# Performance work log

Hardware: AMD Instinct MI355X
Metric: run time of the kernel (lower is better)

## Reference

```python
import jax, jax.numpy as jnp
import numpy as np

E, H, NGRAM, TM, B, NB = 1024, 16, 2, 512, 4, 32


def setup_inputs() -> dict:
    key = jax.random.key(0)
    ks = jax.random.split(key, 12)
    T3 = (NGRAM + 1) * TM
    s = 0.02
    d = {}
    d["hidden_states"] = jax.random.normal(ks[0], (T3, B, E), jnp.float32)
    d["self_attn_mask"] = jax.random.normal(ks[1], (TM, TM), jnp.float32)
    d["ngram_mask_matrix"] = jax.random.normal(ks[2], (NGRAM, 1, TM, 2 * TM), jnp.float32)
    d["i_buckets_main_stream"] = jax.random.randint(ks[3], (B, TM, TM), 0, NB, jnp.int32)
    d["i_bucket_relative_stream"] = jax.random.randint(ks[4], (B, TM, 2 * TM), 0, NB, jnp.int32)
    d["Wq"] = jax.random.normal(ks[5], (E, E), jnp.float32) * s
    d["bq"] = jnp.zeros((E,), jnp.float32)
    d["Wk"] = jax.random.normal(ks[6], (E, E), jnp.float32) * s
    d["bk"] = jnp.zeros((E,), jnp.float32)
    d["Wv"] = jax.random.normal(ks[7], (E, E), jnp.float32) * s
    d["bv"] = jnp.zeros((E,), jnp.float32)
    d["Wo"] = jax.random.normal(ks[8], (E, E), jnp.float32) * s
    d["bo"] = jnp.zeros((E,), jnp.float32)
    d["Wr"] = jax.random.normal(ks[9], (NB * H, E), jnp.float32) * s
    d["br"] = jnp.zeros((NB * H,), jnp.float32)
    return d


def _lin(x, W, b):
    return x @ W.T + b


def reference(hidden_states, self_attn_mask, ngram_mask_matrix,
              i_buckets_main_stream, i_bucket_relative_stream,
              Wq, bq, Wk, bk, Wv, bv, Wo, bo, Wr, br):
    T3, Bb, Ee = hidden_states.shape
    hd = Ee // H
    Tm = T3 // (NGRAM + 1)
    BH = Bb * H

    # projections; q is pre-scaled as in the torch module
    q = _lin(hidden_states, Wq, bq) * (hd ** -0.5)
    k = _lin(hidden_states, Wk, bk)
    v = _lin(hidden_states, Wv, bv)
    # (T3, B, E) -> (BH, T3, hd)
    q = q.reshape(T3, BH, hd).transpose(1, 0, 2)
    k = k.reshape(T3, BH, hd).transpose(1, 0, 2)
    v = v.reshape(T3, BH, hd).transpose(1, 0, 2)

    q_parts = jnp.split(q, NGRAM + 1, axis=1)
    k_parts = jnp.split(k, NGRAM + 1, axis=1)
    v_parts = jnp.split(v, NGRAM + 1, axis=1)
    h_parts = jnp.split(hidden_states, NGRAM + 1, axis=0)
    q_main, k_main, v_main, h_main = q_parts[0], k_parts[0], v_parts[0], h_parts[0]

    # ---------- main stream ----------
    aw_main = jnp.einsum('btd,bsd->bts', q_main, k_main)  # (BH, Tm, Tm)

    # relative-position logits: per-query learned bucket logits, gathered by bucket id
    vals = _lin(h_main.transpose(1, 0, 2), Wr, br)          # (B, Tm, NB*H)
    vals = vals.reshape(Bb, Tm, NB, H).transpose(0, 3, 1, 2).reshape(BH, Tm, NB)
    idx = jnp.broadcast_to(i_buckets_main_stream[:, None], (Bb, H, Tm, Tm)).reshape(BH, Tm, Tm)
    aw_main = aw_main + jnp.take_along_axis(vals, idx, axis=2) + self_attn_mask

    probs_main = jax.nn.softmax(aw_main.astype(jnp.float32), axis=-1).astype(aw_main.dtype)
    attn_main = jnp.einsum('bts,bsd->btd', probs_main, v_main)   # (BH, Tm, hd)
    attn_main = attn_main.transpose(1, 0, 2).reshape(Tm, Bb, Ee)
    attn_main = _lin(attn_main, Wo, bo)                           # (Tm, B, E)

    # ---------- ngram streams ----------
    q_ng = jnp.stack(q_parts[1:], 0)                              # (N, BH, Tm, hd)
    k_ng = jnp.stack([jnp.concatenate([k_main, kp], axis=1) for kp in k_parts[1:]], 0)  # (N, BH, 2Tm, hd)
    v_ng = jnp.stack([jnp.concatenate([v_main, vp], axis=1) for vp in v_parts[1:]], 0)
    h_ng = jnp.stack(h_parts[1:], 0)                              # (N, Tm, B, E)

    aw_ng = jnp.einsum('nbtc,nbsc->nbts', q_ng, k_ng)             # (N, BH, Tm, 2Tm)

    vals_ng = _lin(h_ng.transpose(0, 2, 1, 3), Wr, br)            # (N, B, Tm, NB*H)
    vals_ng = vals_ng.reshape(NGRAM, Bb, Tm, NB, H).transpose(0, 1, 4, 2, 3).reshape(NGRAM, BH, Tm, NB)
    idx_ng = jnp.broadcast_to(i_bucket_relative_stream[None, :, None],
                              (NGRAM, Bb, H, Tm, 2 * Tm)).reshape(NGRAM, BH, Tm, 2 * Tm)
    aw_ng = aw_ng + jnp.take_along_axis(vals_ng, idx_ng, axis=-1) + ngram_mask_matrix

    probs_ng = jax.nn.softmax(aw_ng.astype(jnp.float32), axis=-1).astype(aw_ng.dtype)
    attn_ng = jnp.einsum('nbts,nbsc->nbtc', probs_ng, v_ng)       # (N, BH, Tm, hd)
    attn_ng = attn_ng.transpose(0, 2, 1, 3).reshape(NGRAM, Tm, Bb, Ee)
    attn_ng = _lin(attn_ng, Wo, bo)                                # (N, Tm, B, E)

    attn = jnp.concatenate([attn_main[None], attn_ng], axis=0).reshape(T3, Bb, Ee)
    return attn
```

## Files before the change

kernel.cpp:

```cpp
#include <hip/hip_runtime.h>
#include <hip/hip_fp16.h>
#include <cstdint>

#define T3   1536
#define TMQ  512
#define BB   4
#define EE   1024
#define HH   16
#define HD   64
#define NBK  32
#define BHH  64

#define LOG2E 1.44269504f
#define SM_SHIFT 4.0f

typedef _Float16 half8 __attribute__((ext_vector_type(8)));
typedef float    f32x4 __attribute__((ext_vector_type(4)));

#define SWZ(r, o) ((o) ^ (((r) & 7) << 4))

__device__ inline void gl_lds16(const void* g, void* l) {
    __builtin_amdgcn_global_load_lds(
        (const __attribute__((address_space(1))) uint32_t*)g,
        (__attribute__((address_space(3))) uint32_t*)l, 16, 0, 0);
}

#define VM_WAIT4() asm volatile("s_waitcnt vmcnt(4)" ::: "memory")
#define VM_WAIT0() asm volatile("s_waitcnt vmcnt(0)" ::: "memory")
#define BARRIER()  __builtin_amdgcn_s_barrier()

__global__ __launch_bounds__(256) void cvt_all(
    const float* __restrict__ hs, const float* __restrict__ Wq,
    const float* __restrict__ Wk, const float* __restrict__ Wv,
    const float* __restrict__ Wo, const float* __restrict__ Wr,
    __half* __restrict__ dst)
{
    const long i = (long)blockIdx.x * 256 + threadIdx.x;
    const float* src; long off;
    if (i < 1572864L) { src = hs; off = i; }
    else {
        const long j = i - 1572864L;
        const int  w = (int)(j >> 18);
        const long r = j & 262143L;
        src = (w == 0) ? Wq : (w == 1) ? Wk : (w == 2) ? Wv : (w == 3) ? Wo : Wr;
        off = r;
    }
    const float4 v = ((const float4*)src)[off];
    const __half2 h0 = __floats2half2_rn(v.x, v.y);
    const __half2 h1 = __floats2half2_rn(v.z, v.w);
    uint2 u;
    u.x = *(const unsigned int*)&h0;
    u.y = *(const unsigned int*)&h1;
    ((uint2*)dst)[i] = u;
}

template<int MODE>
__global__ __launch_bounds__(256) void gemm16(
    const __half* __restrict__ A,
    const __half* __restrict__ Wa, const __half* __restrict__ Wb,
    const __half* __restrict__ Wc, const __half* __restrict__ Wd,
    const float* __restrict__ ba, const float* __restrict__ bb,
    const float* __restrict__ bc, const float* __restrict__ bd,
    void* __restrict__ oa, void* __restrict__ ob,
    void* __restrict__ oc, void* __restrict__ od)
{
    __shared__ __half As0[128 * 32], Bs0[128 * 32];
    __shared__ __half As1[128 * 32], Bs1[128 * 32];

    const int tid  = threadIdx.x;
    const int w    = tid >> 6, lane = tid & 63;
    const int m0   = blockIdx.y * 128;

    const __half* Wsel; const float* bsel; void* osel;
    float scale, offs; int n0; int sel = 0;
    if (MODE == 0) {
        const int bx = blockIdx.x;
        sel  = (bx < 24) ? (bx >> 3) : 3;
        n0   = (bx < 24) ? (bx & 7) * 128 : (bx - 24) * 128;
        Wsel = sel == 0 ? Wa : (sel == 1 ? Wb : (sel == 2 ? Wc : Wd));
        bsel = sel == 0 ? ba : (sel == 1 ? bb : (sel == 2 ? bc : bd));
        osel = sel == 0 ? oa : (sel == 1 ? ob : (sel == 2 ? oc : od));
        scale = (sel == 0) ? 0.125f * LOG2E : (sel == 3 ? LOG2E : 1.0f);
        offs  = (sel == 3) ? -SM_SHIFT * LOG2E : 0.0f;
    } else {
        n0 = blockIdx.x * 128; Wsel = Wa; bsel = ba; osel = oa;
        scale = 1.0f; offs = 0.0f;
    }

    f32x4 acc[4][4];
    #pragma unroll
    for (int i = 0; i < 4; ++i)
        #pragma unroll
        for (int j = 0; j < 4; ++j) acc[i][j] = (f32x4){0.f, 0.f, 0.f, 0.f};

    const int wr = w >> 1, wc = w & 1;
    const int lrow = lane & 15, lkg = lane >> 4;
    const int aoff  = (wr * 64 + lrow) * 64;
    const int boff  = (wc * 64 + lrow) * 64;
    const int kbase = (((lkg + ((lrow & 7) >> 1)) & 3) << 4);

    const int stb0 = w * 2048, stb1 = w * 2048 + 1024;
    const int off0 = stb0 + lane * 16, off1 = stb1 + lane * 16;
    const int srow0 = off0 >> 6, srow1 = off1 >> 6;
    const int scol0 = (((((off0 >> 4) & 3) - ((srow0 & 7) >> 1)) & 3) << 4);
    const int scol1 = (((((off1 >> 4) & 3) - ((srow1 & 7) >> 1)) & 3) << 4);
    const char* Ab  = (const char*)A;
    const char* Wb8 = (const char*)Wsel;

#define STAGEK(AS, BS, K0) do {                                                   \
    gl_lds16(Ab  + (size_t)(m0 + srow0) * 2048 + (size_t)(K0) * 2 + scol0,        \
             (char*)(AS) + stb0);                                                 \
    gl_lds16(Wb8 + (size_t)(n0 + srow0) * 2048 + (size_t)(K0) * 2 + scol0,        \
             (char*)(BS) + stb0);                                                 \
    gl_lds16(Ab  + (size_t)(m0 + srow1) * 2048 + (size_t)(K0) * 2 + scol1,        \
             (char*)(AS) + stb1);                                                 \
    gl_lds16(Wb8 + (size_t)(n0 + srow1) * 2048 + (size_t)(K0) * 2 + scol1,        \
             (char*)(BS) + stb1);                                                 \
} while (0)

#define COMPUTEK(AS, BS) do {                                                     \
    half8 af[4], bf[4];                                                           \
    _Pragma("unroll")                                                             \
    for (int m = 0; m < 4; ++m)                                                   \
        af[m] = *(const half8*)((const char*)(AS) + aoff + m * 1024 + kbase);     \
    _Pragma("unroll")                                                             \
    for (int n = 0; n < 4; ++n)                                                   \
        bf[n] = *(const half8*)((const char*)(BS) + boff + n * 1024 + kbase);     \
    _Pragma("unroll")                                                             \
    for (int m = 0; m < 4; ++m)                                                   \
        _Pragma("unroll")                                                         \
        for (int n = 0; n < 4; ++n)                                               \
            acc[m][n] = __builtin_amdgcn_mfma_f32_16x16x32_f16(af[m], bf[n],      \
                                                               acc[m][n], 0, 0, 0);\
} while (0)

    STAGEK(As0, Bs0, 0);

    #pragma unroll 1
    for (int t = 0; t < 16; ++t) {
        const int k0 = t * 64;
        STAGEK(As1, Bs1, k0 + 32);
        VM_WAIT4();
        BARRIER();
        COMPUTEK(As0, Bs0);
        BARRIER();
        if (t < 15) { STAGEK(As0, Bs0, k0 + 64); VM_WAIT4(); }
        else        { VM_WAIT0(); }
        BARRIER();
        COMPUTEK(As1, Bs1);
        BARRIER();
    }

#undef STAGEK
#undef COMPUTEK

    const int col_l  = lane & 15;
    const int row_l4 = (lane >> 4) * 4;
    #pragma unroll
    for (int n = 0; n < 4; ++n) {
        const int gcol = n0 + wc * 64 + n * 16 + col_l;
        const float bias = bsel[gcol];
        #pragma unroll
        for (int m = 0; m < 4; ++m) {
            #pragma unroll
            for (int j = 0; j < 4; ++j) {
                const int grow = m0 + wr * 64 + m * 16 + row_l4 + j;
                const float cval = (acc[m][n][j] + bias) * scale + offs;
                if (MODE == 0) {
                    const int t3 = grow >> 2, bb2 = grow & 3;
                    if (sel == 3) {
                        const int st = t3 >> 9, tm = t3 & 511;
                        const int nb = gcol >> 4, hh2 = gcol & 15;
                        ((float*)osel)[(((size_t)(st * BHH + bb2 * HH + hh2)) * TMQ + tm) * NBK + nb] = cval;
                    } else {
                        const int hh2 = gcol >> 6, d = gcol & 63;
                        __half* oh = (__half*)osel;
                        const __half hv = __float2half(cval);
                        if (sel == 2)
                            oh[((size_t)((bb2 * HH + hh2) * HD + d)) * T3 + t3] = hv;
                        else
                            oh[(((size_t)(bb2 * HH + hh2)) * T3 + t3) * HD + d] = hv;
                    }
                } else {
                    ((float*)osel)[(size_t)grow * EE + gcol] = cval;
                }
            }
        }
    }
}

__global__ __launch_bounds__(256) void attn_mfma(
    const __half* __restrict__ q, const __half* __restrict__ k,
    const __half* __restrict__ vt, const float* __restrict__ vals,
    const float* __restrict__ self_mask, const float* __restrict__ ngram_mask,
    const int* __restrict__ ibm, const int* __restrict__ ibr,
    __half* __restrict__ attn_pre)
{
    __shared__ __half QP [64 * 64];
    __shared__ __half Ks [64 * 64];
    __shared__ __half Vts[64 * 64];
    __shared__ float  vals_s[64 * NBK];

    const int bid = blockIdx.x;
    const int xcd = bid & 7, rr = bid >> 3;
    int s, bh, qt;
    if (rr < 128) { const int g = xcd * 128 + rr; s = 1 + (g >> 9); bh = (g >> 3) & 63; qt = g & 7; }
    else          { const int mi = xcd * 64 + (rr - 128); s = 0; bh = mi >> 3; qt = mi & 7; }
    const int b = bh >> 4, h = bh & 15;
    const int tid = threadIdx.x;
    const int w = tid >> 6, lane = tid & 63;
    const int lc = lane & 15, lg = lane >> 4;
    const int nch = (s == 0) ? 8 : 16;

    {
        const char* qg = (const char*)(q + ((size_t)bh * T3 + s * TMQ + qt * 64) * HD);
        const char* vg = (const char*)(vals + (((size_t)s * BHH + bh) * TMQ + qt * 64) * NBK);
        #pragma unroll
        for (int p = 0; p < 2; ++p) {
            const int u = tid + p * 256;
            const int row = u >> 3, sub = (u & 7) * 16;
            *(uint4*)((char*)QP + row * 128 + SWZ(row, sub)) = *(const uint4*)(qg + (size_t)u * 16);
            *(uint4*)((char*)vals_s + (size_t)u * 16)        = *(const uint4*)(vg + (size_t)u * 16);
        }
    }

    uint4 ku0, ku1, vu0, vu1;
    int   ix[4][4];
    float mk[4][4];
    {
        const char* kg = (const char*)(k + (size_t)bh * T3 * HD);
        const char* vg = (const char*)(vt + (size_t)bh * HD * T3);
        ku0 = *(const uint4*)(kg + (size_t)tid * 16);
        ku1 = *(const uint4*)(kg + (size_t)(tid + 256) * 16);
        vu0 = *(const uint4*)(vg + (size_t)(tid >> 3) * (T3 * 2) + (tid & 7) * 16);
        vu1 = *(const uint4*)(vg + (size_t)((tid + 256) >> 3) * (T3 * 2) + (tid & 7) * 16);
        #pragma unroll
        for (int j = 0; j < 4; ++j) {
            const int t = qt * 64 + w * 16 + lg * 4 + j;
            const int* ip; const float* mp;
            if (s == 0) { ip = ibm + ((size_t)b * TMQ + t) * TMQ + lc;
                          mp = self_mask + (size_t)t * TMQ + lc; }
            else        { ip = ibr + ((size_t)b * TMQ + t) * (2 * TMQ) + lc;
                          mp = ngram_mask + ((size_t)(s - 1) * TMQ + t) * (2 * TMQ) + lc; }
            #pragma unroll
            for (int n = 0; n < 4; ++n) { ix[j][n] = ip[n * 16]; mk[j][n] = mp[n * 16]; }
        }
    }
    __syncthreads();

    half8 aq[2];
    {
        const int qr = w * 16 + lc;
        const char* qb = (const char*)QP + qr * 128;
        aq[0] = *(const half8*)(qb + SWZ(qr, lg * 16));
        aq[1] = *(const half8*)(qb + SWZ(qr, 64 + lg * 16));
    }

    f32x4 o[4];
    #pragma unroll
    for (int nd = 0; nd < 4; ++nd) o[nd] = (f32x4){0.f, 0.f, 0.f, 0.f};
    float l_p[4] = {0.f, 0.f, 0.f, 0.f};

    for (int c = 0; c < nch; ++c) {
        if (c > 0) __syncthreads();
        {
            const int u0 = tid, u1 = tid + 256;
            const int r0 = u0 >> 3, s0 = (u0 & 7) * 16;
            const int r1 = u1 >> 3, s1 = (u1 & 7) * 16;
            *(uint4*)((char*)Ks  + r0 * 128 + SWZ(r0, s0)) = ku0;
            *(uint4*)((char*)Ks  + r1 * 128 + SWZ(r1, s1)) = ku1;
            *(uint4*)((char*)Vts + r0 * 128 + SWZ(r0, s0)) = vu0;
            *(uint4*)((char*)Vts + r1 * 128 + SWZ(r1, s1)) = vu1;
        }
        __syncthreads();

        if (c + 1 < nch) {
            const int jn  = (c + 1) * 64;
            const int t3n = (jn < TMQ) ? jn : s * TMQ + (jn - TMQ);
            const char* kg = (const char*)(k + ((size_t)bh * T3 + t3n) * HD);
            const char* vg = (const char*)(vt + (size_t)bh * HD * T3 + t3n);
            ku0 = *(const uint4*)(kg + (size_t)tid * 16);
            ku1 = *(const uint4*)(kg + (size_t)(tid + 256) * 16);
            vu0 = *(const uint4*)(vg + (size_t)(tid >> 3) * (T3 * 2) + (tid & 7) * 16);
            vu1 = *(const uint4*)(vg + (size_t)((tid + 256) >> 3) * (T3 * 2) + (tid & 7) * 16);
        }

        f32x4 sc[4];
        #pragma unroll
        for (int n = 0; n < 4; ++n) sc[n] = (f32x4){0.f, 0.f, 0.f, 0.f};
        __builtin_amdgcn_s_setprio(1);
        #pragma unroll
        for (int ks = 0; ks < 2; ++ks) {
            #pragma unroll
            for (int n = 0; n < 4; ++n) {
                const int kr = n * 16 + lc;
                const half8 bk = *(const half8*)((const char*)Ks + kr * 128 + SWZ(kr, ks * 64 + lg * 16));
                sc[n] = __builtin_amdgcn_mfma_f32_16x16x32_f16(aq[ks], bk, sc[n], 0, 0, 0);
            }
        }
        __builtin_amdgcn_s_setprio(0);

        #pragma unroll
        for (int j = 0; j < 4; ++j) {
            const int ql = w * 16 + lg * 4 + j;
            const float* vr = vals_s + ql * NBK;
            float p[4];
            #pragma unroll
            for (int n = 0; n < 4; ++n) {
                const float sv = fmaf(mk[j][n], LOG2E, sc[n][j] + vr[ix[j][n]]);
                p[n] = __builtin_amdgcn_exp2f(sv);
            }
            l_p[j] += (p[0] + p[1]) + (p[2] + p[3]);
            char* pb = (char*)QP + ql * 128;
            *(__half*)(pb + SWZ(ql, (0 * 16 + lc) * 2)) = __float2half(p[0]);
            *(__half*)(pb + SWZ(ql, (1 * 16 + lc) * 2)) = __float2half(p[1]);
            *(__half*)(pb + SWZ(ql, (2 * 16 + lc) * 2)) = __float2half(p[2]);
            *(__half*)(pb + SWZ(ql, (3 * 16 + lc) * 2)) = __float2half(p[3]);
        }

        if (c + 1 < nch) {
            const int jn = (c + 1) * 64;
            #pragma unroll
            for (int j = 0; j < 4; ++j) {
                const int t = qt * 64 + w * 16 + lg * 4 + j;
                const int* ip; const float* mp;
                if (s == 0) { ip = ibm + ((size_t)b * TMQ + t) * TMQ + jn + lc;
                              mp = self_mask + (size_t)t * TMQ + jn + lc; }
                else        { ip = ibr + ((size_t)b * TMQ + t) * (2 * TMQ) + jn + lc;
                              mp = ngram_mask + ((size_t)(s - 1) * TMQ + t) * (2 * TMQ) + jn + lc; }
                #pragma unroll
                for (int n = 0; n < 4; ++n) { ix[j][n] = ip[n * 16]; mk[j][n] = mp[n * 16]; }
            }
        }
        __threadfence_block();

        __builtin_amdgcn_s_setprio(1);
        #pragma unroll
        for (int ks = 0; ks < 2; ++ks) {
            const int ar = w * 16 + lc;
            const half8 ap = *(const half8*)((const char*)QP + ar * 128 + SWZ(ar, ks * 64 + lg * 16));
            #pragma unroll
            for (int nd = 0; nd < 4; ++nd) {
                const int vr2 = nd * 16 + lc;
                const half8 bv = *(const half8*)((const char*)Vts + vr2 * 128 + SWZ(vr2, ks * 64 + lg * 16));
                o[nd] = __builtin_amdgcn_mfma_f32_16x16x32_f16(ap, bv, o[nd], 0, 0, 0);
            }
        }
        __builtin_amdgcn_s_setprio(0);
    }

    #pragma unroll
    for (int j = 0; j < 4; ++j) {
        float l = l_p[j];
        l += __shfl_xor(l, 1);
        l += __shfl_xor(l, 2);
        l += __shfl_xor(l, 4);
        l += __shfl_xor(l, 8);
        const float inv = 1.0f / l;
        const int t = qt * 64 + w * 16 + lg * 4 + j;
        __half* op = attn_pre + (((size_t)(s * TMQ + t)) * BB + b) * EE + h * HD + lc;
        #pragma unroll
        for (int nd = 0; nd < 4; ++nd)
            op[nd * 16] = __float2half(o[nd][j] * inv);
    }
}

extern "C" void kernel_launch(void* const* d_in, const int* in_sizes, int n_in,
                              void* d_out, int out_size, void* d_ws, size_t ws_size,
                              hipStream_t stream)
{
    const float* hs    = (const float*)d_in[0];
    const float* smask = (const float*)d_in[1];
    const float* nmask = (const float*)d_in[2];
    const int*   ibm   = (const int*)d_in[3];
    const int*   ibr   = (const int*)d_in[4];
    const float* Wq = (const float*)d_in[5];
    const float* bq = (const float*)d_in[6];
    const float* Wk = (const float*)d_in[7];
    const float* bk = (const float*)d_in[8];
    const float* Wv = (const float*)d_in[9];
    const float* bv = (const float*)d_in[10];
    const float* Wo = (const float*)d_in[11];
    const float* bo = (const float*)d_in[12];
    const float* Wr = (const float*)d_in[13];
    const float* br = (const float*)d_in[14];
    float* out = (float*)d_out;

    const size_t NQKV = (size_t)BHH * T3 * HD;
    __half* qh    = (__half*)d_ws;
    __half* kh    = qh + NQKV;
    __half* vth   = kh + NQKV;
    float*  valsw = (float*)(vth + NQKV);
    __half* hs_h  = (__half*)(valsw + (size_t)3 * BHH * TMQ * NBK);
    __half* apre_h = hs_h;
    __half* Wq_h = hs_h + (size_t)T3 * BB * EE;
    __half* Wk_h = Wq_h + (size_t)EE * EE;
    __half* Wv_h = Wk_h + (size_t)EE * EE;
    __half* Wo_h = Wv_h + (size_t)EE * EE;
    __half* Wr_h = Wo_h + (size_t)EE * EE;

    dim3 blk(256);
    cvt_all<<<dim3(10752), blk, 0, stream>>>(hs, Wq, Wk, Wv, Wo, Wr, hs_h);

    gemm16<0><<<dim3(28, 48), blk, 0, stream>>>(hs_h, Wq_h, Wk_h, Wv_h, Wr_h,
                                                bq, bk, bv, br,
                                                qh, kh, vth, valsw);
    attn_mfma<<<dim3(1536), blk, 0, stream>>>(qh, kh, vth, valsw, smask, nmask,
                                              ibm, ibr, apre_h);
    gemm16<2><<<dim3(8, 48), blk, 0, stream>>>(apre_h, Wo_h, nullptr, nullptr, nullptr,
                                               bo, nullptr, nullptr, nullptr,
                                               out, nullptr, nullptr, nullptr);
}
```

Baseline: 211.9 us.

## Triple-buffer GEMM K-loop, remap blocks per XCD, and double attention query tile

The projection GEMMs move from a two-stage to a three-stage LDS ring, keeping two K-slices in flight, and raise wave priority around the MFMA block. GEMM block indices are remapped so consecutive row tiles land on the same XCD for L2 reuse of the weight tiles. The attention kernel now processes 128 query rows per block with 512 threads, halving the grid so each K/V chunk loaded into LDS is shared by twice as many queries. The cost is more LDS per block, which may lower occupancy, and fewer blocks to spread across the CUs.

```diff
diff --git a/kernel.cpp b/kernel.cpp
--- a/kernel.cpp
+++ b/kernel.cpp
@@ -25,6 +25,7 @@
         (__attribute__((address_space(3))) uint32_t*)l, 16, 0, 0);
 }
 
+#define VM_WAIT8() asm volatile("s_waitcnt vmcnt(8)" ::: "memory")
 #define VM_WAIT4() asm volatile("s_waitcnt vmcnt(4)" ::: "memory")
 #define VM_WAIT0() asm volatile("s_waitcnt vmcnt(0)" ::: "memory")
 #define BARRIER()  __builtin_amdgcn_s_barrier()
@@ -66,15 +67,21 @@
 {
     __shared__ __half As0[128 * 32], Bs0[128 * 32];
     __shared__ __half As1[128 * 32], Bs1[128 * 32];
+    __shared__ __half As2[128 * 32], Bs2[128 * 32];
 
     const int tid  = threadIdx.x;
     const int w    = tid >> 6, lane = tid & 63;
-    const int m0   = blockIdx.y * 128;
+
+    const int GX   = (MODE == 0) ? 28 : 8;
+    const int bidl = blockIdx.x + GX * blockIdx.y;
+    const int xcd  = bidl & 7, idx = bidl >> 3;
+    const int bx   = idx % GX;
+    const int by   = (idx / GX) * 8 + xcd;
+    const int m0   = by * 128;
 
     const __half* Wsel; const float* bsel; void* osel;
     float scale, offs; int n0; int sel = 0;
     if (MODE == 0) {
-        const int bx = blockIdx.x;
         sel  = (bx < 24) ? (bx >> 3) : 3;
         n0   = (bx < 24) ? (bx & 7) * 128 : (bx - 24) * 128;
         Wsel = sel == 0 ? Wa : (sel == 1 ? Wb : (sel == 2 ? Wc : Wd));
@@ -83,7 +90,7 @@
         scale = (sel == 0) ? 0.125f * LOG2E : (sel == 3 ? LOG2E : 1.0f);
         offs  = (sel == 3) ? -SM_SHIFT * LOG2E : 0.0f;
     } else {
-        n0 = blockIdx.x * 128; Wsel = Wa; bsel = ba; osel = oa;
+        n0 = bx * 128; Wsel = Wa; bsel = ba; osel = oa;
         scale = 1.0f; offs = 0.0f;
     }
 
@@ -126,30 +133,33 @@
     _Pragma("unroll")                                                             \
     for (int n = 0; n < 4; ++n)                                                   \
         bf[n] = *(const half8*)((const char*)(BS) + boff + n * 1024 + kbase);     \
+    __builtin_amdgcn_s_setprio(1);                                                \
     _Pragma("unroll")                                                             \
     for (int m = 0; m < 4; ++m)                                                   \
         _Pragma("unroll")                                                         \
         for (int n = 0; n < 4; ++n)                                               \
             acc[m][n] = __builtin_amdgcn_mfma_f32_16x16x32_f16(af[m], bf[n],      \
                                                                acc[m][n], 0, 0, 0);\
+    __builtin_amdgcn_s_setprio(0);                                                \
 } while (0)
 
     STAGEK(As0, Bs0, 0);
+    STAGEK(As1, Bs1, 32);
 
     #pragma unroll 1
-    for (int t = 0; t < 16; ++t) {
-        const int k0 = t * 64;
-        STAGEK(As1, Bs1, k0 + 32);
-        VM_WAIT4();
-        BARRIER();
-        COMPUTEK(As0, Bs0);
-        BARRIER();
-        if (t < 15) { STAGEK(As0, Bs0, k0 + 64); VM_WAIT4(); }
-        else        { VM_WAIT0(); }
-        BARRIER();
-        COMPUTEK(As1, Bs1);
-        BARRIER();
-    }
+    for (int it = 0; it < 10; ++it) {
+        const int kb0 = it * 96;
+        STAGEK(As2, Bs2, kb0 + 64);  VM_WAIT8(); BARRIER();
+        COMPUTEK(As0, Bs0);          BARRIER();
+        STAGEK(As0, Bs0, kb0 + 96);  VM_WAIT8(); BARRIER();
+        COMPUTEK(As1, Bs1);          BARRIER();
+        STAGEK(As1, Bs1, kb0 + 128); VM_WAIT8(); BARRIER();
+        COMPUTEK(As2, Bs2);          BARRIER();
+    }
+    VM_WAIT4(); BARRIER();
+    COMPUTEK(As0, Bs0);
+    VM_WAIT0(); BARRIER();
+    COMPUTEK(As1, Bs1);
 
 #undef STAGEK
 #undef COMPUTEK
@@ -189,23 +199,23 @@
     }
 }
 
-__global__ __launch_bounds__(256) void attn_mfma(
+__global__ __launch_bounds__(512) void attn_mfma(
     const __half* __restrict__ q, const __half* __restrict__ k,
     const __half* __restrict__ vt, const float* __restrict__ vals,
     const float* __restrict__ self_mask, const float* __restrict__ ngram_mask,
     const int* __restrict__ ibm, const int* __restrict__ ibr,
     __half* __restrict__ attn_pre)
 {
-    __shared__ __half QP [64 * 64];
+    __shared__ __half QP [128 * 64];
     __shared__ __half Ks [64 * 64];
     __shared__ __half Vts[64 * 64];
-    __shared__ float  vals_s[64 * NBK];
+    __shared__ float  vals_s[128 * NBK];
 
     const int bid = blockIdx.x;
     const int xcd = bid & 7, rr = bid >> 3;
     int s, bh, qt;
-    if (rr < 128) { const int g = xcd * 128 + rr; s = 1 + (g >> 9); bh = (g >> 3) & 63; qt = g & 7; }
-    else          { const int mi = xcd * 64 + (rr - 128); s = 0; bh = mi >> 3; qt = mi & 7; }
+    if (rr < 64) { const int g = xcd * 64 + rr; s = 1 + (g >> 8); bh = (g >> 2) & 63; qt = g & 3; }
+    else         { const int mi = xcd * 32 + (rr - 64); s = 0; bh = mi >> 2; qt = mi & 3; }
     const int b = bh >> 4, h = bh & 15;
     const int tid = threadIdx.x;
     const int w = tid >> 6, lane = tid & 63;
@@ -213,30 +223,28 @@
     const int nch = (s == 0) ? 8 : 16;
 
     {
-        const char* qg = (const char*)(q + ((size_t)bh * T3 + s * TMQ + qt * 64) * HD);
-        const char* vg = (const char*)(vals + (((size_t)s * BHH + bh) * TMQ + qt * 64) * NBK);
+        const char* qg = (const char*)(q + ((size_t)bh * T3 + s * TMQ + qt * 128) * HD);
+        const char* vg = (const char*)(vals + (((size_t)s * BHH + bh) * TMQ + qt * 128) * NBK);
         #pragma unroll
         for (int p = 0; p < 2; ++p) {
-            const int u = tid + p * 256;
+            const int u = tid + p * 512;
             const int row = u >> 3, sub = (u & 7) * 16;
             *(uint4*)((char*)QP + row * 128 + SWZ(row, sub)) = *(const uint4*)(qg + (size_t)u * 16);
             *(uint4*)((char*)vals_s + (size_t)u * 16)        = *(const uint4*)(vg + (size_t)u * 16);
         }
     }
 
-    uint4 ku0, ku1, vu0, vu1;
+    uint4 ku0, vu0;
     int   ix[4][4];
     float mk[4][4];
     {
         const char* kg = (const char*)(k + (size_t)bh * T3 * HD);
         const char* vg = (const char*)(vt + (size_t)bh * HD * T3);
         ku0 = *(const uint4*)(kg + (size_t)tid * 16);
-        ku1 = *(const uint4*)(kg + (size_t)(tid + 256) * 16);
         vu0 = *(const uint4*)(vg + (size_t)(tid >> 3) * (T3 * 2) + (tid & 7) * 16);
-        vu1 = *(const uint4*)(vg + (size_t)((tid + 256) >> 3) * (T3 * 2) + (tid & 7) * 16);
         #pragma unroll
         for (int j = 0; j < 4; ++j) {
-            const int t = qt * 64 + w * 16 + lg * 4 + j;
+            const int t = qt * 128 + w * 16 + lg * 4 + j;
             const int* ip; const float* mp;
             if (s == 0) { ip = ibm + ((size_t)b * TMQ + t) * TMQ + lc;
                           mp = self_mask + (size_t)t * TMQ + lc; }
@@ -264,13 +272,9 @@
     for (int c = 0; c < nch; ++c) {
         if (c > 0) __syncthreads();
         {
-            const int u0 = tid, u1 = tid + 256;
-            const int r0 = u0 >> 3, s0 = (u0 & 7) * 16;
-            const int r1 = u1 >> 3, s1 = (u1 & 7) * 16;
+            const int r0 = tid >> 3, s0 = (tid & 7) * 16;
             *(uint4*)((char*)Ks  + r0 * 128 + SWZ(r0, s0)) = ku0;
-            *(uint4*)((char*)Ks  + r1 * 128 + SWZ(r1, s1)) = ku1;
             *(uint4*)((char*)Vts + r0 * 128 + SWZ(r0, s0)) = vu0;
-            *(uint4*)((char*)Vts + r1 * 128 + SWZ(r1, s1)) = vu1;
         }
         __syncthreads();
 
@@ -280,9 +284,7 @@
             const char* kg = (const char*)(k + ((size_t)bh * T3 + t3n) * HD);
             const char* vg = (const char*)(vt + (size_t)bh * HD * T3 + t3n);
             ku0 = *(const uint4*)(kg + (size_t)tid * 16);
-            ku1 = *(const uint4*)(kg + (size_t)(tid + 256) * 16);
             vu0 = *(const uint4*)(vg + (size_t)(tid >> 3) * (T3 * 2) + (tid & 7) * 16);
-            vu1 = *(const uint4*)(vg + (size_t)((tid + 256) >> 3) * (T3 * 2) + (tid & 7) * 16);
         }
 
         f32x4 sc[4];
@@ -322,7 +324,7 @@
             const int jn = (c + 1) * 64;
             #pragma unroll
             for (int j = 0; j < 4; ++j) {
-                const int t = qt * 64 + w * 16 + lg * 4 + j;
+                const int t = qt * 128 + w * 16 + lg * 4 + j;
                 const int* ip; const float* mp;
                 if (s == 0) { ip = ibm + ((size_t)b * TMQ + t) * TMQ + jn + lc;
                               mp = self_mask + (size_t)t * TMQ + jn + lc; }
@@ -357,7 +359,7 @@
         l += __shfl_xor(l, 4);
         l += __shfl_xor(l, 8);
         const float inv = 1.0f / l;
-        const int t = qt * 64 + w * 16 + lg * 4 + j;
+        const int t = qt * 128 + w * 16 + lg * 4 + j;
         __half* op = attn_pre + (((size_t)(s * TMQ + t)) * BB + b) * EE + h * HD + lc;
         #pragma unroll
         for (int nd = 0; nd < 4; ++nd)
@@ -405,8 +407,8 @@
     gemm16<0><<<dim3(28, 48), blk, 0, stream>>>(hs_h, Wq_h, Wk_h, Wv_h, Wr_h,
                                                 bq, bk, bv, br,
                                                 qh, kh, vth, valsw);
-    attn_mfma<<<dim3(1536), blk, 0, stream>>>(qh, kh, vth, valsw, smask, nmask,
-                                              ibm, ibr, apre_h);
+    attn_mfma<<<dim3(768), dim3(512), 0, stream>>>(qh, kh, vth, valsw, smask, nmask,
+                                                   ibm, ibr, apre_h);
     gemm16<2><<<dim3(8, 48), blk, 0, stream>>>(apre_h, Wo_h, nullptr, nullptr, nullptr,
                                                bo, nullptr, nullptr, nullptr,
                                                out, nullptr, nullptr, nullptr);
```

Measured after the change: 207.8 us. Within noise of the previous version (-1.9%).
